# Kernel tuning notes

Hardware: AMD Instinct MI355X
Metric: run time of the kernel (lower is better)

The kernel has to match this reference:

```python
import jax, jax.numpy as jnp
import numpy as np

B, S, H = 4, 1024, 1024
NH, HD = 16, 64          # num_head, head_dim = embd/num_head
L = 256                  # latent_dim
RD, RH = 64, 32          # rope_dim, rope_half
DF = 2048                # d_ff
E, K = 8, 2              # num_experts, top_k
LN_EPS = 1e-5


def _ln(x, g, b):
    m = x.mean(-1, keepdims=True)
    v = ((x - m) ** 2).mean(-1, keepdims=True)
    return (x - m) / jnp.sqrt(v + LN_EPS) * g + b


def _rope(x, cos, sin):
    # interleaved rope: even/odd pairs, matching torch even=x[...,0::2]
    xe, xo = x[..., 0::2], x[..., 1::2]
    re = xe * cos - xo * sin
    ro = xe * sin + xo * cos
    return jnp.stack([re, ro], axis=-1).reshape(x.shape)


def setup_inputs() -> dict:
    key = jax.random.key(0)
    ks = jax.random.split(key, 16)
    sd = 0.02
    return {
        "x": jax.random.normal(ks[0], (B, S, H), jnp.float32),
        "ln1_g": jnp.ones((H,), jnp.float32),
        "ln1_b": jnp.zeros((H,), jnp.float32),
        "W_ckv": jax.random.normal(ks[1], (H, L), jnp.float32) * sd,
        "W_kv": jax.random.normal(ks[2], (L, 2 * H), jnp.float32) * sd,
        "W_cq": jax.random.normal(ks[3], (H, L), jnp.float32) * sd,
        "W_q": jax.random.normal(ks[4], (L, H), jnp.float32) * sd,
        "W_qr": jax.random.normal(ks[5], (L, NH * RD), jnp.float32) * sd,
        "W_kr": jax.random.normal(ks[6], (L, RD), jnp.float32) * sd,
        "W_o": jax.random.normal(ks[7], (H, H), jnp.float32) * sd,
        "ln2_g": jnp.ones((H,), jnp.float32),
        "ln2_b": jnp.zeros((H,), jnp.float32),
        "centroids": jax.random.normal(ks[8], (E, H), jnp.float32),
        "routing_bias": jnp.zeros((E,), jnp.float32),
        "Wg": jax.random.normal(ks[9], (E, H, DF), jnp.float32) * sd,
        "Wu": jax.random.normal(ks[10], (E, H, DF), jnp.float32) * sd,
        "Wd": jax.random.normal(ks[11], (E, DF, H), jnp.float32) * sd,
    }


def reference(x, ln1_g, ln1_b, W_ckv, W_kv, W_cq, W_q, W_qr, W_kr, W_o,
              ln2_g, ln2_b, centroids, routing_bias, Wg, Wu, Wd):
    # ---- MLA attention ----
    h1 = _ln(x, ln1_g, ln1_b)
    c_kv = h1 @ W_ckv                       # [B,S,L]
    kv = c_kv @ W_kv                        # [B,S,2H]
    c_q = h1 @ W_cq                         # [B,S,L]
    q_c = (c_q @ W_q).reshape(B, S, NH, HD).transpose(0, 2, 1, 3)
    q_r = (c_q @ W_qr).reshape(B, S, NH, RD).transpose(0, 2, 1, 3)
    k_r = (c_kv @ W_kr)[:, None, :, :]      # [B,1,S,RD] shared across heads
    k_c, v = jnp.split(kv, 2, axis=-1)
    k_c = k_c.reshape(B, S, NH, HD).transpose(0, 2, 1, 3)
    v = v.reshape(B, S, NH, HD).transpose(0, 2, 1, 3)

    pos = jnp.arange(S, dtype=jnp.float32)
    inv_freq = 1.0 / (10000.0 ** (jnp.arange(0, RD, 2, dtype=jnp.float32) / RD))
    fr = pos[:, None] * inv_freq            # [S,RH]
    cos, sin = jnp.cos(fr)[None, None], jnp.sin(fr)[None, None]
    q_r = _rope(q_r, cos, sin)
    k_r = jnp.broadcast_to(_rope(k_r, cos, sin), (B, NH, S, RD))

    q = jnp.concatenate([q_c, q_r], axis=-1)   # [B,NH,S,HD+RD]
    k = jnp.concatenate([k_c, k_r], axis=-1)
    scale = HD ** -0.5                         # module uses head_dim scale
    scores = jnp.einsum('bhqd,bhkd->bhqk', q, k) * scale
    causal = jnp.tril(jnp.ones((S, S), bool))
    scores = jnp.where(causal, scores, -jnp.inf)
    attn = jax.nn.softmax(scores, axis=-1)
    o = jnp.einsum('bhqk,bhkd->bhqd', attn, v).transpose(0, 2, 1, 3).reshape(B, S, H)
    x = x + o @ W_o

    # ---- MoE FFN ----
    xf = _ln(x, ln2_g, ln2_b).reshape(-1, H)   # [T,H]
    aff = jax.nn.sigmoid(xf @ centroids.T)     # [T,E]
    biased = aff + routing_bias
    tk_s, tk_i = jax.lax.top_k(biased, K)      # [T,K]
    tk_w = jax.nn.softmax(tk_s, axis=-1)
    counts = jnp.sum(jax.nn.one_hot(tk_i, E, dtype=jnp.int32), axis=(0, 1))

    out = jnp.zeros_like(xf)
    for e in range(E):  # fixed small loop over structurally distinct experts
        we = jnp.sum(tk_w * (tk_i == e), axis=-1)           # combine weight per token
        hh = jax.nn.silu(xf @ Wg[e]) * (xf @ Wu[e])
        out = out + we[:, None] * (hh @ Wd[e])
    x = x + out.reshape(B, S, H)
    return x, counts
```

## Files before the change

### kernel.cpp

```cpp
#include <hip/hip_runtime.h>
#include <hip/hip_bf16.h>
#include <math.h>

#define SEQ 1024
#define HDIM 1024
#define NHEAD 16
#define HEADD 64
#define LDIM 256
#define RDIM 64
#define DFF 2048
#define NEXP 8
#define ROWS 4096

typedef __attribute__((ext_vector_type(8))) short short8;
typedef __attribute__((ext_vector_type(4))) float f32x4;

static __device__ __forceinline__ short f2bf_s(float v) {
    __hip_bfloat16 hb = __float2bfloat16(v);
    return *reinterpret_cast<short*>(&hb);
}

__global__ __launch_bounds__(256) void ln_kernel(const float* __restrict__ x,
                                                 const float* __restrict__ g,
                                                 const float* __restrict__ b,
                                                 float* __restrict__ out_f,
                                                 __hip_bfloat16* __restrict__ out_bf) {
    int row = blockIdx.x;
    int tid = threadIdx.x;
    __shared__ float red[256];
    __shared__ float red2[256];
    const float* xr = x + (size_t)row * HDIM;
    float s = 0.f, s2 = 0.f;
    for (int j = tid; j < HDIM; j += 256) { float v = xr[j]; s += v; s2 += v * v; }
    red[tid] = s; red2[tid] = s2; __syncthreads();
    for (int o = 128; o > 0; o >>= 1) {
        if (tid < o) { red[tid] += red[tid + o]; red2[tid] += red2[tid + o]; }
        __syncthreads();
    }
    float mean = red[0] * (1.f / HDIM);
    float var = red2[0] * (1.f / HDIM) - mean * mean;
    float inv = rsqrtf(var + 1e-5f);
    for (int j = tid; j < HDIM; j += 256) {
        float v = (xr[j] - mean) * inv * g[j] + b[j];
        if (out_f) out_f[(size_t)row * HDIM + j] = v;
        if (out_bf) out_bf[(size_t)row * HDIM + j] = __float2bfloat16(v);
    }
}

__global__ __launch_bounds__(256) void transpose_bf16_kernel(const float* __restrict__ src,
                                                             __hip_bfloat16* __restrict__ dst,
                                                             int K, int N, float scale) {
    int n0 = blockIdx.x * 64, k0 = blockIdx.y * 64;
    size_t eo = (size_t)blockIdx.z * K * N;
    src += eo; dst += eo;
    __shared__ float t[64][65];
    int tid = threadIdx.x;
    #pragma unroll
    for (int i = 0; i < 16; i++) {
        int id = tid + i * 256;
        int r = id >> 6, cn = id & 63;
        t[r][cn] = src[(size_t)(k0 + r) * N + n0 + cn];
    }
    __syncthreads();
    #pragma unroll
    for (int i = 0; i < 16; i++) {
        int id = tid + i * 256;
        int rn = id >> 6, ck = id & 63;
        dst[(size_t)(n0 + rn) * K + k0 + ck] = __float2bfloat16(t[ck][rn] * scale);
    }
}

__global__ __launch_bounds__(256) void cvt_bf16_kernel(const float* __restrict__ src,
                                                       __hip_bfloat16* __restrict__ dst) {
    int i = (blockIdx.x * 256 + threadIdx.x) * 4;
    float4 v = *(const float4*)(src + i);
    union { unsigned long long u; __hip_bfloat16 b[4]; } cv;
    cv.b[0] = __float2bfloat16(v.x);
    cv.b[1] = __float2bfloat16(v.y);
    cv.b[2] = __float2bfloat16(v.z);
    cv.b[3] = __float2bfloat16(v.w);
    *(unsigned long long*)(dst + i) = cv.u;
}

__global__ __launch_bounds__(256) void gemm_bf16_kernel(const __hip_bfloat16* __restrict__ A,
                                                        const __hip_bfloat16* __restrict__ Bt,
                                                        float* __restrict__ Cf,
                                                        __hip_bfloat16* __restrict__ Cbf,
                                                        const float* __restrict__ R,
                                                        int M, int N, int K, int mode) {
    int m0 = blockIdx.y * 128, n0 = blockIdx.x * 128;
    __shared__ short As[128 * 64];
    __shared__ short Bs[128 * 64];
    int tid = threadIdx.x;
    int lane = tid & 63, w = tid >> 6;
    int wr = w >> 1, wc = w & 1;
    int lm = lane & 15, g = lane >> 4;
    f32x4 acc[4][4] = {};
    for (int k0 = 0; k0 < K; k0 += 64) {
        #pragma unroll
        for (int rr = 0; rr < 4; rr++) {
            int cid = tid + rr * 256;
            int row = cid >> 3, p = cid & 7;
            int c = p ^ (row & 7);
            *(short8*)(&As[cid * 8]) = *(const short8*)((const short*)A + (size_t)(m0 + row) * K + k0 + c * 8);
            *(short8*)(&Bs[cid * 8]) = *(const short8*)((const short*)Bt + (size_t)(n0 + row) * K + k0 + c * 8);
        }
        __syncthreads();
        #pragma unroll
        for (int kk = 0; kk < 2; kk++) {
            short8 a[4], bv[4];
            #pragma unroll
            for (int i = 0; i < 4; i++) {
                int row = wr * 64 + i * 16 + lm;
                int c = (kk * 4 + g) ^ (row & 7);
                a[i] = *(const short8*)(&As[row * 64 + c * 8]);
            }
            #pragma unroll
            for (int j = 0; j < 4; j++) {
                int row = wc * 64 + j * 16 + lm;
                int c = (kk * 4 + g) ^ (row & 7);
                bv[j] = *(const short8*)(&Bs[row * 64 + c * 8]);
            }
            #pragma unroll
            for (int i = 0; i < 4; i++)
                #pragma unroll
                for (int j = 0; j < 4; j++)
                    acc[i][j] = __builtin_amdgcn_mfma_f32_16x16x32_bf16(a[i], bv[j], acc[i][j], 0, 0, 0);
        }
        __syncthreads();
    }
    #pragma unroll
    for (int i = 0; i < 4; i++) {
        #pragma unroll
        for (int r = 0; r < 4; r++) {
            int m = m0 + wr * 64 + i * 16 + g * 4 + r;
            #pragma unroll
            for (int j = 0; j < 4; j++) {
                int n = n0 + wc * 64 + j * 16 + lm;
                float v = acc[i][j][r];
                if (mode == 0) {
                    size_t idx = (size_t)m * N + n;
                    if (R) v += R[idx];
                    if (Cf) Cf[idx] = v;
                    if (Cbf) Cbf[idx] = __float2bfloat16(v);
                } else {
                    size_t idx = ((size_t)((m >> 10) * 16 + (n >> 6)) * SEQ + (m & 1023)) * 128
                               + (n & 63) + (mode == 2 ? 64 : 0);
                    Cbf[idx] = __float2bfloat16(v);
                }
            }
        }
    }
}

__global__ __launch_bounds__(256) void gemm_kr_kernel(const __hip_bfloat16* __restrict__ A,
                                                      const __hip_bfloat16* __restrict__ Bt,
                                                      __hip_bfloat16* __restrict__ C) {
    int m0 = blockIdx.x * 64;
    int tid = threadIdx.x;
    int lane = tid & 63, w = tid >> 6;
    int lm = lane & 15, g = lane >> 4;
    f32x4 acc[4] = {};
    const short* Ab = (const short*)A + (size_t)(m0 + w * 16 + lm) * 256;
    #pragma unroll
    for (int ks = 0; ks < 8; ks++) {
        short8 a = *(const short8*)(Ab + ks * 32 + g * 8);
        #pragma unroll
        for (int j = 0; j < 4; j++) {
            short8 b = *(const short8*)((const short*)Bt + (size_t)(j * 16 + lm) * 256 + ks * 32 + g * 8);
            acc[j] = __builtin_amdgcn_mfma_f32_16x16x32_bf16(a, b, acc[j], 0, 0, 0);
        }
    }
    #pragma unroll
    for (int r = 0; r < 4; r++)
        #pragma unroll
        for (int j = 0; j < 4; j++)
            C[(size_t)(m0 + w * 16 + g * 4 + r) * 64 + j * 16 + lm] = __float2bfloat16(acc[j][r]);
}

__global__ void rope_q_kernel(__hip_bfloat16* __restrict__ q_bf) {
    int idx = blockIdx.x * 256 + threadIdx.x;
    int i = idx & 31;
    int s = (idx >> 5) & 1023;
    int bh = idx >> 15;
    float freq = __expf(-9.210340372f * (float)i / 32.f);
    float fr = (float)s * freq;
    float sn, cs;
    __sincosf(fr, &sn, &cs);
    __hip_bfloat16* p = q_bf + ((size_t)bh * SEQ + s) * 128 + 64 + 2 * i;
    float xe = __bfloat162float(p[0]), xo = __bfloat162float(p[1]);
    p[0] = __float2bfloat16(xe * cs - xo * sn);
    p[1] = __float2bfloat16(xe * sn + xo * cs);
}

__global__ void rope_pack_kr_kernel(const __hip_bfloat16* __restrict__ k_r_bf,
                                    __hip_bfloat16* __restrict__ k_bf) {
    int idx = blockIdx.x * 256 + threadIdx.x;
    int i = idx & 31;
    int row = idx >> 5;
    int s = row & 1023, b = row >> 10;
    float freq = __expf(-9.210340372f * (float)i / 32.f);
    float fr = (float)s * freq;
    float sn, cs;
    __sincosf(fr, &sn, &cs);
    float xe = __bfloat162float(k_r_bf[(size_t)row * 64 + 2 * i]);
    float xo = __bfloat162float(k_r_bf[(size_t)row * 64 + 2 * i + 1]);
    __hip_bfloat16 re = __float2bfloat16(xe * cs - xo * sn);
    __hip_bfloat16 ro = __float2bfloat16(xe * sn + xo * cs);
    #pragma unroll
    for (int h = 0; h < NHEAD; h++) {
        size_t base = ((size_t)(b * 16 + h) * SEQ + s) * 128 + 64 + 2 * i;
        k_bf[base] = re;
        k_bf[base + 1] = ro;
    }
}

__global__ __launch_bounds__(256) void pack_vt_kernel(const __hip_bfloat16* __restrict__ v_bf,
                                                      __hip_bfloat16* __restrict__ vt_bf) {
    int s0 = blockIdx.x * 64, h = blockIdx.y, b = blockIdx.z;
    __shared__ short t[64][72];
    int tid = threadIdx.x;
    #pragma unroll
    for (int i = 0; i < 16; i++) {
        int id = tid + i * 256;
        int r = id >> 6, d = id & 63;
        t[r][d] = ((const short*)v_bf)[(size_t)(b * SEQ + s0 + r) * HDIM + h * 64 + d];
    }
    __syncthreads();
    #pragma unroll
    for (int i = 0; i < 16; i++) {
        int id = tid + i * 256;
        int d = id >> 6, cs = id & 63;
        ((short*)vt_bf)[((size_t)(b * 16 + h) * 64 + d) * SEQ + s0 + cs] = t[cs][d];
    }
}

__global__ __launch_bounds__(256) void attn_mfma_kernel(const __hip_bfloat16* __restrict__ q_bf,
                                                        const __hip_bfloat16* __restrict__ k_bf,
                                                        const __hip_bfloat16* __restrict__ vt_bf,
                                                        __hip_bfloat16* __restrict__ obuf) {
    int qt = blockIdx.x, h = blockIdx.y, b = blockIdx.z;
    int bh = b * NHEAD + h;
    int tid = threadIdx.x;
    int lane = tid & 63, w = tid >> 6;
    int lm = lane & 15, g = lane >> 4;
    __shared__ short Ks[64 * 128];
    __shared__ short Vts[64 * 64];
    __shared__ short Ps[64 * 64];
    short8 aq[4];
    const short* qbase = (const short*)q_bf + ((size_t)bh * SEQ + qt * 64 + w * 16 + lm) * 128;
    #pragma unroll
    for (int st = 0; st < 4; st++) aq[st] = *(const short8*)(qbase + st * 32 + g * 8);
    f32x4 oacc[4] = {};
    float mrow[4], lrow[4];
    #pragma unroll
    for (int r = 0; r < 4; r++) { mrow[r] = -1e30f; lrow[r] = 0.f; }
    const short* kb = (const short*)k_bf + (size_t)bh * SEQ * 128;
    const short* vb = (const short*)vt_bf + (size_t)bh * 64 * SEQ;

    for (int kt = 0; kt <= qt; kt++) {
        __syncthreads();
        #pragma unroll
        for (int it = 0; it < 4; it++) {
            int cid = tid + it * 256;
            int row = cid >> 4, p = cid & 15;
            int c = p ^ (row & 15);
            *(short8*)(&Ks[row * 128 + p * 8]) = *(const short8*)(kb + (size_t)(kt * 64 + row) * 128 + c * 8);
        }
        #pragma unroll
        for (int it = 0; it < 2; it++) {
            int cid = tid + it * 256;
            int row = cid >> 3, p = cid & 7;
            int c = p ^ (row & 7);
            *(short8*)(&Vts[row * 64 + p * 8]) = *(const short8*)(vb + (size_t)row * SEQ + kt * 64 + c * 8);
        }
        __syncthreads();
        f32x4 s[4] = {};
        #pragma unroll
        for (int st = 0; st < 4; st++) {
            #pragma unroll
            for (int j = 0; j < 4; j++) {
                int row = j * 16 + lm;
                int q = (st * 4 + g) ^ (row & 15);
                short8 bk = *(const short8*)(&Ks[row * 128 + q * 8]);
                s[j] = __builtin_amdgcn_mfma_f32_16x16x32_bf16(aq[st], bk, s[j], 0, 0, 0);
            }
        }
        if (kt == qt) {
            #pragma unroll
            for (int j = 0; j < 4; j++)
                #pragma unroll
                for (int r = 0; r < 4; r++)
                    if (j * 16 + lm > w * 16 + g * 4 + r) s[j][r] = -1e30f;
        }
        float fac[4];
        #pragma unroll
        for (int r = 0; r < 4; r++) {
            float mx = fmaxf(fmaxf(s[0][r], s[1][r]), fmaxf(s[2][r], s[3][r]));
            mx = fmaxf(mx, __shfl_xor(mx, 1));
            mx = fmaxf(mx, __shfl_xor(mx, 2));
            mx = fmaxf(mx, __shfl_xor(mx, 4));
            mx = fmaxf(mx, __shfl_xor(mx, 8));
            float mnew = fmaxf(mrow[r], mx);
            float ps = 0.f;
            #pragma unroll
            for (int j = 0; j < 4; j++) {
                float pv = __expf(s[j][r] - mnew);
                s[j][r] = pv;
                ps += pv;
            }
            ps += __shfl_xor(ps, 1);
            ps += __shfl_xor(ps, 2);
            ps += __shfl_xor(ps, 4);
            ps += __shfl_xor(ps, 8);
            fac[r] = __expf(mrow[r] - mnew);
            lrow[r] = lrow[r] * fac[r] + ps;
            mrow[r] = mnew;
        }
        #pragma unroll
        for (int j2 = 0; j2 < 4; j2++)
            #pragma unroll
            for (int r = 0; r < 4; r++) oacc[j2][r] *= fac[r];
        #pragma unroll
        for (int j = 0; j < 4; j++) {
            #pragma unroll
            for (int r = 0; r < 4; r++) {
                int rowl = w * 16 + g * 4 + r;
                int col = j * 16 + lm;
                int ch = (col >> 3) ^ (rowl & 7);
                Ps[rowl * 64 + ch * 8 + (col & 7)] = f2bf_s(s[j][r]);
            }
        }
        __syncthreads();
        #pragma unroll
        for (int st = 0; st < 2; st++) {
            int rowp = w * 16 + lm;
            int qp = (st * 4 + g) ^ (rowp & 7);
            short8 ap = *(const short8*)(&Ps[rowp * 64 + qp * 8]);
            #pragma unroll
            for (int j2 = 0; j2 < 4; j2++) {
                int rowv = j2 * 16 + lm;
                int qv = (st * 4 + g) ^ (rowv & 7);
                short8 bv = *(const short8*)(&Vts[rowv * 64 + qv * 8]);
                oacc[j2] = __builtin_amdgcn_mfma_f32_16x16x32_bf16(ap, bv, oacc[j2], 0, 0, 0);
            }
        }
    }
    #pragma unroll
    for (int r = 0; r < 4; r++) {
        float inv = 1.f / lrow[r];
        size_t rowg = (size_t)b * SEQ + qt * 64 + w * 16 + g * 4 + r;
        #pragma unroll
        for (int j2 = 0; j2 < 4; j2++)
            obuf[rowg * HDIM + h * 64 + j2 * 16 + lm] = __float2bfloat16(oacc[j2][r] * inv);
    }
}

__global__ void init_kernel(int* counts, int* pos) {
    int t = threadIdx.x;
    if (t < NEXP) { counts[t] = 0; pos[t] = 0; }
}

__global__ __launch_bounds__(64) void route_kernel(const float* __restrict__ xf,
                                                   const float* __restrict__ cent,
                                                   const float* __restrict__ rbias,
                                                   int* __restrict__ route_i,
                                                   float* __restrict__ route_w,
                                                   int* __restrict__ counts) {
    int row = blockIdx.x;
    int lane = threadIdx.x;
    const float* xr = xf + (size_t)row * HDIM;
    float p[NEXP] = {};
    for (int j = lane; j < HDIM; j += 64) {
        float xv = xr[j];
        for (int e = 0; e < NEXP; e++) p[e] += xv * cent[e * HDIM + j];
    }
    for (int e = 0; e < NEXP; e++) {
        float v = p[e];
        for (int o = 32; o > 0; o >>= 1) v += __shfl_down(v, o);
        p[e] = v;
    }
    if (lane == 0) {
        float biased[NEXP];
        for (int e = 0; e < NEXP; e++) {
            float aff = 1.f / (1.f + expf(-p[e]));
            biased[e] = aff + rbias[e];
        }
        int i0 = 0; float v0 = biased[0];
        for (int e = 1; e < NEXP; e++) if (biased[e] > v0) { v0 = biased[e]; i0 = e; }
        int i1 = -1; float v1 = -1e30f;
        for (int e = 0; e < NEXP; e++) if (e != i0 && biased[e] > v1) { v1 = biased[e]; i1 = e; }
        float e1 = expf(v1 - v0);
        float wsum = 1.f + e1;
        route_i[row * 2] = i0; route_i[row * 2 + 1] = i1;
        route_w[row * 2] = 1.f / wsum; route_w[row * 2 + 1] = e1 / wsum;
        atomicAdd(&counts[i0], 1);
        atomicAdd(&counts[i1], 1);
    }
}

__global__ void offsets_kernel(const int* counts, int* eoff, float* out_counts) {
    int acc = 0;
    for (int e = 0; e < NEXP; e++) { eoff[e] = acc; acc += counts[e]; out_counts[e] = (float)counts[e]; }
    eoff[NEXP] = acc;
}

__global__ void scatter_kernel(const int* route_i, const float* route_w, const int* eoff,
                               int* pos, int* tok_id, float* tok_w) {
    int row = blockIdx.x * 256 + threadIdx.x;
    if (row >= ROWS) return;
    for (int sl = 0; sl < 2; sl++) {
        int e = route_i[row * 2 + sl];
        int p = atomicAdd(&pos[e], 1);
        int dst = eoff[e] + p;
        tok_id[dst] = row;
        tok_w[dst] = route_w[row * 2 + sl];
    }
}

__global__ __launch_bounds__(256) void moe_gu_mfma(const __hip_bfloat16* __restrict__ xf_bf,
                                                   const __hip_bfloat16* __restrict__ Wg_t,
                                                   const __hip_bfloat16* __restrict__ Wu_t,
                                                   const int* __restrict__ counts,
                                                   const int* __restrict__ eoff,
                                                   const int* __restrict__ tok_id,
                                                   __hip_bfloat16* __restrict__ hh) {
    int e = blockIdx.z;
    int n_e = counts[e];
    int t0 = blockIdx.y * 128;
    if (t0 >= n_e) return;
    int n0 = blockIdx.x * 64;
    __shared__ short As[128 * 64];
    __shared__ short Bgs[64 * 64];
    __shared__ short Bus[64 * 64];
    __shared__ int toks[128];
    int tid = threadIdx.x;
    int lane = tid & 63, w = tid >> 6;
    int wr = w >> 1, wc = w & 1;
    if (tid < 128) {
        int idx = t0 + tid;
        toks[tid] = (idx < n_e) ? tok_id[eoff[e] + idx] : 0;
    }
    __syncthreads();
    f32x4 accg[4][2] = {};
    f32x4 accu[4][2] = {};
    const __hip_bfloat16* Wge = Wg_t + (size_t)e * DFF * HDIM;
    const __hip_bfloat16* Wue = Wu_t + (size_t)e * DFF * HDIM;
    for (int k0 = 0; k0 < HDIM; k0 += 64) {
        #pragma unroll
        for (int rr = 0; rr < 4; rr++) {
            int chunk = tid + rr * 256;
            int row = chunk >> 3, p = chunk & 7;
            int c = p ^ (row & 7);
            *(short8*)(&As[chunk * 8]) =
                *(const short8*)((const short*)xf_bf + (size_t)toks[row] * HDIM + k0 + c * 8);
        }
        #pragma unroll
        for (int rr = 0; rr < 2; rr++) {
            int chunk = tid + rr * 256;
            int row = chunk >> 3, p = chunk & 7;
            int c = p ^ (row & 7);
            *(short8*)(&Bgs[chunk * 8]) =
                *(const short8*)((const short*)Wge + (size_t)(n0 + row) * HDIM + k0 + c * 8);
            *(short8*)(&Bus[chunk * 8]) =
                *(const short8*)((const short*)Wue + (size_t)(n0 + row) * HDIM + k0 + c * 8);
        }
        __syncthreads();
        #pragma unroll
        for (int kk = 0; kk < 2; kk++) {
            short8 a[4], bg[2], bu[2];
            #pragma unroll
            for (int i = 0; i < 4; i++) {
                int row = wr * 64 + i * 16 + (lane & 15);
                int c = (kk * 4 + (lane >> 4)) ^ (row & 7);
                a[i] = *(const short8*)(&As[row * 64 + c * 8]);
            }
            #pragma unroll
            for (int j = 0; j < 2; j++) {
                int row = wc * 32 + j * 16 + (lane & 15);
                int c = (kk * 4 + (lane >> 4)) ^ (row & 7);
                bg[j] = *(const short8*)(&Bgs[row * 64 + c * 8]);
                bu[j] = *(const short8*)(&Bus[row * 64 + c * 8]);
            }
            #pragma unroll
            for (int i = 0; i < 4; i++)
                #pragma unroll
                for (int j = 0; j < 2; j++) {
                    accg[i][j] = __builtin_amdgcn_mfma_f32_16x16x32_bf16(a[i], bg[j], accg[i][j], 0, 0, 0);
                    accu[i][j] = __builtin_amdgcn_mfma_f32_16x16x32_bf16(a[i], bu[j], accu[i][j], 0, 0, 0);
                }
        }
        __syncthreads();
    }
    #pragma unroll
    for (int i = 0; i < 4; i++) {
        #pragma unroll
        for (int r = 0; r < 4; r++) {
            int row = wr * 64 + i * 16 + (lane >> 4) * 4 + r;
            if (t0 + row < n_e) {
                size_t slot = (size_t)eoff[e] + t0 + row;
                #pragma unroll
                for (int j = 0; j < 2; j++) {
                    float gv = accg[i][j][r];
                    float uv = accu[i][j][r];
                    float val = gv / (1.f + __expf(-gv)) * uv;
                    hh[slot * DFF + n0 + wc * 32 + j * 16 + (lane & 15)] = __float2bfloat16(val);
                }
            }
        }
    }
}

__global__ __launch_bounds__(256) void moe_down_mfma(const __hip_bfloat16* __restrict__ hh,
                                                     const __hip_bfloat16* __restrict__ Wd_t,
                                                     const int* __restrict__ counts,
                                                     const int* __restrict__ eoff,
                                                     const int* __restrict__ tok_id,
                                                     const float* __restrict__ tok_w,
                                                     float* __restrict__ out) {
    int e = blockIdx.z;
    int n_e = counts[e];
    int t0 = blockIdx.y * 128;
    if (t0 >= n_e) return;
    int n0 = blockIdx.x * 128;
    __shared__ short As[128 * 64];
    __shared__ short Bs[128 * 64];
    int tid = threadIdx.x;
    int lane = tid & 63, w = tid >> 6;
    int wr = w >> 1, wc = w & 1;
    f32x4 acc[4][4] = {};
    const __hip_bfloat16* Ae = hh + (size_t)(eoff[e] + t0) * DFF;
    const __hip_bfloat16* Be = Wd_t + (size_t)e * HDIM * DFF;
    for (int k0 = 0; k0 < DFF; k0 += 64) {
        #pragma unroll
        for (int rr = 0; rr < 4; rr++) {
            int chunk = tid + rr * 256;
            int row = chunk >> 3, p = chunk & 7;
            int c = p ^ (row & 7);
            *(short8*)(&As[chunk * 8]) =
                *(const short8*)((const short*)Ae + (size_t)row * DFF + k0 + c * 8);
            *(short8*)(&Bs[chunk * 8]) =
                *(const short8*)((const short*)Be + (size_t)(n0 + row) * DFF + k0 + c * 8);
        }
        __syncthreads();
        #pragma unroll
        for (int kk = 0; kk < 2; kk++) {
            short8 a[4], bv[4];
            #pragma unroll
            for (int i = 0; i < 4; i++) {
                int row = wr * 64 + i * 16 + (lane & 15);
                int c = (kk * 4 + (lane >> 4)) ^ (row & 7);
                a[i] = *(const short8*)(&As[row * 64 + c * 8]);
            }
            #pragma unroll
            for (int j = 0; j < 4; j++) {
                int row = wc * 64 + j * 16 + (lane & 15);
                int c = (kk * 4 + (lane >> 4)) ^ (row & 7);
                bv[j] = *(const short8*)(&Bs[row * 64 + c * 8]);
            }
            #pragma unroll
            for (int i = 0; i < 4; i++)
                #pragma unroll
                for (int j = 0; j < 4; j++)
                    acc[i][j] = __builtin_amdgcn_mfma_f32_16x16x32_bf16(a[i], bv[j], acc[i][j], 0, 0, 0);
        }
        __syncthreads();
    }
    #pragma unroll
    for (int i = 0; i < 4; i++) {
        #pragma unroll
        for (int r = 0; r < 4; r++) {
            int row = wr * 64 + i * 16 + (lane >> 4) * 4 + r;
            if (t0 + row < n_e) {
                int slot = eoff[e] + t0 + row;
                int tok = tok_id[slot];
                float tw = tok_w[slot];
                #pragma unroll
                for (int j = 0; j < 4; j++) {
                    int col = n0 + wc * 64 + j * 16 + (lane & 15);
                    atomicAdd(&out[(size_t)tok * HDIM + col], tw * acc[i][j][r]);
                }
            }
        }
    }
}

extern "C" void kernel_launch(void* const* d_in, const int* in_sizes, int n_in,
                              void* d_out, int out_size, void* d_ws, size_t ws_size,
                              hipStream_t stream) {
    const float* x = (const float*)d_in[0];
    const float* ln1_g = (const float*)d_in[1];
    const float* ln1_b = (const float*)d_in[2];
    const float* W_ckv = (const float*)d_in[3];
    const float* W_kv = (const float*)d_in[4];
    const float* W_cq = (const float*)d_in[5];
    const float* W_q = (const float*)d_in[6];
    const float* W_qr = (const float*)d_in[7];
    const float* W_kr = (const float*)d_in[8];
    const float* W_o = (const float*)d_in[9];
    const float* ln2_g = (const float*)d_in[10];
    const float* ln2_b = (const float*)d_in[11];
    const float* cent = (const float*)d_in[12];
    const float* rbias = (const float*)d_in[13];
    const float* Wg = (const float*)d_in[14];
    const float* Wu = (const float*)d_in[15];
    const float* Wd = (const float*)d_in[16];
    float* out = (float*)d_out;

    float* ws = (float*)d_ws;
    __hip_bfloat16* h1_bf   = (__hip_bfloat16*)ws;
    __hip_bfloat16* c_kv_bf = h1_bf + (size_t)ROWS * HDIM;
    __hip_bfloat16* c_q_bf  = c_kv_bf + (size_t)ROWS * LDIM;
    __hip_bfloat16* k_r_bf  = c_q_bf + (size_t)ROWS * LDIM;
    __hip_bfloat16* q_bf    = k_r_bf + (size_t)ROWS * RDIM;
    __hip_bfloat16* k_bf    = q_bf + (size_t)ROWS * 2048;
    __hip_bfloat16* v_bf    = k_bf + (size_t)ROWS * 2048;
    __hip_bfloat16* vt_bf   = v_bf + (size_t)ROWS * HDIM;
    __hip_bfloat16* obuf_bf = vt_bf + (size_t)ROWS * HDIM;
    __hip_bfloat16* Wckv_t  = obuf_bf + (size_t)ROWS * HDIM;
    __hip_bfloat16* Wcq_t   = Wckv_t + 1024 * 256;
    __hip_bfloat16* Wkv_t   = Wcq_t + 1024 * 256;
    __hip_bfloat16* Wq_t    = Wkv_t + 2048 * 256;
    __hip_bfloat16* Wqr_t   = Wq_t + 1024 * 256;
    __hip_bfloat16* Wo_t    = Wqr_t + 1024 * 256;
    __hip_bfloat16* Wkr_t   = Wo_t + 1024 * 1024;
    __hip_bfloat16* Wg_t  = (__hip_bfloat16*)ws;
    __hip_bfloat16* Wu_t  = Wg_t + (size_t)NEXP * DFF * HDIM;
    __hip_bfloat16* Wd_t  = Wu_t + (size_t)NEXP * DFF * HDIM;
    __hip_bfloat16* xf_bf = Wd_t + (size_t)NEXP * DFF * HDIM;
    float* xf = ws + ((size_t)3 * NEXP * DFF * HDIM + (size_t)ROWS * HDIM) / 2;
    __hip_bfloat16* hh = (__hip_bfloat16*)xf;
    float* tail = xf + (size_t)(2 * ROWS + 128) * DFF / 2;
    float* route_w = tail;
    float* tok_w = tail + ROWS * 2;
    int* ibuf = (int*)(tok_w + ROWS * 2);
    int* route_i = ibuf;
    int* counts = ibuf + 8192;
    int* eoff = ibuf + 8200;
    int* pos = ibuf + 8212;
    int* tok_id = ibuf + 8224;

    ln_kernel<<<ROWS, 256, 0, stream>>>(x, ln1_g, ln1_b, nullptr, h1_bf);
    transpose_bf16_kernel<<<dim3(4, 16, 1), 256, 0, stream>>>(W_ckv, Wckv_t, 1024, 256, 1.f);
    transpose_bf16_kernel<<<dim3(4, 16, 1), 256, 0, stream>>>(W_cq, Wcq_t, 1024, 256, 1.f);
    transpose_bf16_kernel<<<dim3(32, 4, 1), 256, 0, stream>>>(W_kv, Wkv_t, 256, 2048, 1.f);
    transpose_bf16_kernel<<<dim3(16, 4, 1), 256, 0, stream>>>(W_q, Wq_t, 256, 1024, 0.125f);
    transpose_bf16_kernel<<<dim3(16, 4, 1), 256, 0, stream>>>(W_qr, Wqr_t, 256, 1024, 0.125f);
    transpose_bf16_kernel<<<dim3(16, 16, 1), 256, 0, stream>>>(W_o, Wo_t, 1024, 1024, 1.f);
    transpose_bf16_kernel<<<dim3(1, 4, 1), 256, 0, stream>>>(W_kr, Wkr_t, 256, 64, 1.f);
    gemm_bf16_kernel<<<dim3(2, 32), 256, 0, stream>>>(h1_bf, Wckv_t, nullptr, c_kv_bf, nullptr, ROWS, 256, 1024, 0);
    gemm_bf16_kernel<<<dim3(2, 32), 256, 0, stream>>>(h1_bf, Wcq_t, nullptr, c_q_bf, nullptr, ROWS, 256, 1024, 0);
    gemm_bf16_kernel<<<dim3(8, 32), 256, 0, stream>>>(c_kv_bf, Wkv_t, nullptr, k_bf, nullptr, ROWS, 1024, 256, 1);
    gemm_bf16_kernel<<<dim3(8, 32), 256, 0, stream>>>(c_kv_bf, Wkv_t + 1024 * 256, nullptr, v_bf, nullptr, ROWS, 1024, 256, 0);
    gemm_bf16_kernel<<<dim3(8, 32), 256, 0, stream>>>(c_q_bf, Wq_t, nullptr, q_bf, nullptr, ROWS, 1024, 256, 1);
    gemm_bf16_kernel<<<dim3(8, 32), 256, 0, stream>>>(c_q_bf, Wqr_t, nullptr, q_bf, nullptr, ROWS, 1024, 256, 2);
    gemm_kr_kernel<<<64, 256, 0, stream>>>(c_kv_bf, Wkr_t, k_r_bf);
    rope_q_kernel<<<(4 * 16 * 1024 * 32) / 256, 256, 0, stream>>>(q_bf);
    rope_pack_kr_kernel<<<(ROWS * 32) / 256, 256, 0, stream>>>(k_r_bf, k_bf);
    pack_vt_kernel<<<dim3(16, 16, 4), 256, 0, stream>>>(v_bf, vt_bf);
    attn_mfma_kernel<<<dim3(SEQ / 64, NHEAD, 4), 256, 0, stream>>>(q_bf, k_bf, vt_bf, obuf_bf);
    gemm_bf16_kernel<<<dim3(8, 32), 256, 0, stream>>>(obuf_bf, Wo_t, out, nullptr, x, ROWS, 1024, 1024, 0);
    ln_kernel<<<ROWS, 256, 0, stream>>>(out, ln2_g, ln2_b, xf, nullptr);
    transpose_bf16_kernel<<<dim3(32, 16, NEXP), 256, 0, stream>>>(Wg, Wg_t, HDIM, DFF, 1.f);
    transpose_bf16_kernel<<<dim3(32, 16, NEXP), 256, 0, stream>>>(Wu, Wu_t, HDIM, DFF, 1.f);
    transpose_bf16_kernel<<<dim3(16, 32, NEXP), 256, 0, stream>>>(Wd, Wd_t, DFF, HDIM, 1.f);
    cvt_bf16_kernel<<<(ROWS * HDIM / 4) / 256, 256, 0, stream>>>(xf, xf_bf);
    init_kernel<<<1, 64, 0, stream>>>(counts, pos);
    route_kernel<<<ROWS, 64, 0, stream>>>(xf, cent, rbias, route_i, route_w, counts);
    offsets_kernel<<<1, 1, 0, stream>>>(counts, eoff, out + (size_t)ROWS * HDIM);
    scatter_kernel<<<ROWS / 256, 256, 0, stream>>>(route_i, route_w, eoff, pos, tok_id, tok_w);
    moe_gu_mfma<<<dim3(DFF / 64, 32, NEXP), 256, 0, stream>>>(xf_bf, Wg_t, Wu_t, counts, eoff, tok_id, hh);
    moe_down_mfma<<<dim3(HDIM / 128, 32, NEXP), 256, 0, stream>>>(hh, Wd_t, counts, eoff, tok_id, tok_w, out);
}
```

Measured before the change: 918.4 us.

## Use direct global-to-LDS loads in GEMM, attention and MoE kernels; fuse bf16 cast into LN

Global-to-shared tile staging in the dense GEMM, attention K/V loads and both MoE GEMMs now uses the global_load_lds builtin, so data goes straight into LDS without passing through VGPRs. Per-thread token row offsets for the gathered MoE A tile are precomputed once, outside the k loop. The separate fp32-to-bf16 conversion kernel is removed and the second layernorm writes bf16 directly. One __syncthreads between the P writes and P reads in attention is also removed, which looks like it could create a race unless each wave only reads its own P rows.

```diff
diff --git a/kernel.cpp b/kernel.cpp
--- a/kernel.cpp
+++ b/kernel.cpp
@@ -20,6 +20,13 @@
     return *reinterpret_cast<short*>(&hb);
 }
 
+static __device__ __forceinline__ void gload_lds16(const void* g, void* l) {
+    __builtin_amdgcn_global_load_lds(
+        (const __attribute__((address_space(1))) unsigned int*)g,
+        (__attribute__((address_space(3))) unsigned int*)l,
+        16, 0, 0);
+}
+
 __global__ __launch_bounds__(256) void ln_kernel(const float* __restrict__ x,
                                                  const float* __restrict__ g,
                                                  const float* __restrict__ b,
@@ -68,18 +75,6 @@
         int rn = id >> 6, ck = id & 63;
         dst[(size_t)(n0 + rn) * K + k0 + ck] = __float2bfloat16(t[ck][rn] * scale);
     }
-}
-
-__global__ __launch_bounds__(256) void cvt_bf16_kernel(const float* __restrict__ src,
-                                                       __hip_bfloat16* __restrict__ dst) {
-    int i = (blockIdx.x * 256 + threadIdx.x) * 4;
-    float4 v = *(const float4*)(src + i);
-    union { unsigned long long u; __hip_bfloat16 b[4]; } cv;
-    cv.b[0] = __float2bfloat16(v.x);
-    cv.b[1] = __float2bfloat16(v.y);
-    cv.b[2] = __float2bfloat16(v.z);
-    cv.b[3] = __float2bfloat16(v.w);
-    *(unsigned long long*)(dst + i) = cv.u;
 }
 
 __global__ __launch_bounds__(256) void gemm_bf16_kernel(const __hip_bfloat16* __restrict__ A,
@@ -99,11 +94,12 @@
     for (int k0 = 0; k0 < K; k0 += 64) {
         #pragma unroll
         for (int rr = 0; rr < 4; rr++) {
-            int cid = tid + rr * 256;
-            int row = cid >> 3, p = cid & 7;
+            int sb = w * 64 + rr * 256;
+            int slot = sb + lane;
+            int row = slot >> 3, p = slot & 7;
             int c = p ^ (row & 7);
-            *(short8*)(&As[cid * 8]) = *(const short8*)((const short*)A + (size_t)(m0 + row) * K + k0 + c * 8);
-            *(short8*)(&Bs[cid * 8]) = *(const short8*)((const short*)Bt + (size_t)(n0 + row) * K + k0 + c * 8);
+            gload_lds16((const short*)A + (size_t)(m0 + row) * K + k0 + c * 8, &As[sb * 8]);
+            gload_lds16((const short*)Bt + (size_t)(n0 + row) * K + k0 + c * 8, &Bs[sb * 8]);
         }
         __syncthreads();
         #pragma unroll
@@ -262,17 +258,19 @@
         __syncthreads();
         #pragma unroll
         for (int it = 0; it < 4; it++) {
-            int cid = tid + it * 256;
+            int sb = w * 64 + it * 256;
+            int cid = sb + lane;
             int row = cid >> 4, p = cid & 15;
             int c = p ^ (row & 15);
-            *(short8*)(&Ks[row * 128 + p * 8]) = *(const short8*)(kb + (size_t)(kt * 64 + row) * 128 + c * 8);
+            gload_lds16(kb + (size_t)(kt * 64 + row) * 128 + c * 8, &Ks[sb * 8]);
         }
         #pragma unroll
         for (int it = 0; it < 2; it++) {
-            int cid = tid + it * 256;
+            int sb = w * 64 + it * 256;
+            int cid = sb + lane;
             int row = cid >> 3, p = cid & 7;
             int c = p ^ (row & 7);
-            *(short8*)(&Vts[row * 64 + p * 8]) = *(const short8*)(vb + (size_t)row * SEQ + kt * 64 + c * 8);
+            gload_lds16(vb + (size_t)row * SEQ + kt * 64 + c * 8, &Vts[sb * 8]);
         }
         __syncthreads();
         f32x4 s[4] = {};
@@ -331,7 +329,6 @@
                 Ps[rowl * 64 + ch * 8 + (col & 7)] = f2bf_s(s[j][r]);
             }
         }
-        __syncthreads();
         #pragma unroll
         for (int st = 0; st < 2; st++) {
             int rowp = w * 16 + lm;
@@ -442,6 +439,14 @@
         toks[tid] = (idx < n_e) ? tok_id[eoff[e] + idx] : 0;
     }
     __syncthreads();
+    int atok[4], acoff[4];
+    #pragma unroll
+    for (int rr = 0; rr < 4; rr++) {
+        int slot = tid + rr * 256;
+        int row = slot >> 3, p = slot & 7;
+        atok[rr] = toks[row];
+        acoff[rr] = (p ^ (row & 7)) * 8;
+    }
     f32x4 accg[4][2] = {};
     f32x4 accu[4][2] = {};
     const __hip_bfloat16* Wge = Wg_t + (size_t)e * DFF * HDIM;
@@ -449,21 +454,17 @@
     for (int k0 = 0; k0 < HDIM; k0 += 64) {
         #pragma unroll
         for (int rr = 0; rr < 4; rr++) {
-            int chunk = tid + rr * 256;
-            int row = chunk >> 3, p = chunk & 7;
+            int sb = w * 64 + rr * 256;
+            gload_lds16((const short*)xf_bf + (size_t)atok[rr] * HDIM + k0 + acoff[rr], &As[sb * 8]);
+        }
+        #pragma unroll
+        for (int rr = 0; rr < 2; rr++) {
+            int sb = w * 64 + rr * 256;
+            int slot = sb + lane;
+            int row = slot >> 3, p = slot & 7;
             int c = p ^ (row & 7);
-            *(short8*)(&As[chunk * 8]) =
-                *(const short8*)((const short*)xf_bf + (size_t)toks[row] * HDIM + k0 + c * 8);
-        }
-        #pragma unroll
-        for (int rr = 0; rr < 2; rr++) {
-            int chunk = tid + rr * 256;
-            int row = chunk >> 3, p = chunk & 7;
-            int c = p ^ (row & 7);
-            *(short8*)(&Bgs[chunk * 8]) =
-                *(const short8*)((const short*)Wge + (size_t)(n0 + row) * HDIM + k0 + c * 8);
-            *(short8*)(&Bus[chunk * 8]) =
-                *(const short8*)((const short*)Wue + (size_t)(n0 + row) * HDIM + k0 + c * 8);
+            gload_lds16((const short*)Wge + (size_t)(n0 + row) * HDIM + k0 + c * 8, &Bgs[sb * 8]);
+            gload_lds16((const short*)Wue + (size_t)(n0 + row) * HDIM + k0 + c * 8, &Bus[sb * 8]);
         }
         __syncthreads();
         #pragma unroll
@@ -534,13 +535,12 @@
     for (int k0 = 0; k0 < DFF; k0 += 64) {
         #pragma unroll
         for (int rr = 0; rr < 4; rr++) {
-            int chunk = tid + rr * 256;
-            int row = chunk >> 3, p = chunk & 7;
+            int sb = w * 64 + rr * 256;
+            int slot = sb + lane;
+            int row = slot >> 3, p = slot & 7;
             int c = p ^ (row & 7);
-            *(short8*)(&As[chunk * 8]) =
-                *(const short8*)((const short*)Ae + (size_t)row * DFF + k0 + c * 8);
-            *(short8*)(&Bs[chunk * 8]) =
-                *(const short8*)((const short*)Be + (size_t)(n0 + row) * DFF + k0 + c * 8);
+            gload_lds16((const short*)Ae + (size_t)row * DFF + k0 + c * 8, &As[sb * 8]);
+            gload_lds16((const short*)Be + (size_t)(n0 + row) * DFF + k0 + c * 8, &Bs[sb * 8]);
         }
         __syncthreads();
         #pragma unroll
@@ -660,11 +660,10 @@
     pack_vt_kernel<<<dim3(16, 16, 4), 256, 0, stream>>>(v_bf, vt_bf);
     attn_mfma_kernel<<<dim3(SEQ / 64, NHEAD, 4), 256, 0, stream>>>(q_bf, k_bf, vt_bf, obuf_bf);
     gemm_bf16_kernel<<<dim3(8, 32), 256, 0, stream>>>(obuf_bf, Wo_t, out, nullptr, x, ROWS, 1024, 1024, 0);
-    ln_kernel<<<ROWS, 256, 0, stream>>>(out, ln2_g, ln2_b, xf, nullptr);
+    ln_kernel<<<ROWS, 256, 0, stream>>>(out, ln2_g, ln2_b, xf, xf_bf);
     transpose_bf16_kernel<<<dim3(32, 16, NEXP), 256, 0, stream>>>(Wg, Wg_t, HDIM, DFF, 1.f);
     transpose_bf16_kernel<<<dim3(32, 16, NEXP), 256, 0, stream>>>(Wu, Wu_t, HDIM, DFF, 1.f);
     transpose_bf16_kernel<<<dim3(16, 32, NEXP), 256, 0, stream>>>(Wd, Wd_t, DFF, HDIM, 1.f);
-    cvt_bf16_kernel<<<(ROWS * HDIM / 4) / 256, 256, 0, stream>>>(xf, xf_bf);
     init_kernel<<<1, 64, 0, stream>>>(counts, pos);
     route_kernel<<<ROWS, 64, 0, stream>>>(xf, cent, rbias, route_i, route_w, counts);
     offsets_kernel<<<1, 1, 0, stream>>>(counts, eoff, out + (size_t)ROWS * HDIM);
```

Result: faster. 887.5 us (-3.4%).
